# Kernel tuning notes

Measured on AMD Instinct MI355X. Metric: run time of the kernel, lower is better.

The kernel has to match this reference:

```python
import jax, jax.numpy as jnp
import numpy as np

N = 8192       # nodes per graph
E = 262144     # edges per graph (avg degree 32)
D_IN, D_H, D_OUT = 128, 256, 64


def _gcn_layer(x, src, dst, W, b, n):
    # PyG GCNConv: add self-loops, symmetric normalization D^-1/2 (A+I) D^-1/2, then + bias
    xw = x @ W
    loop = jnp.arange(n)
    src_f = jnp.concatenate([src, loop])
    dst_f = jnp.concatenate([dst, loop])
    deg = jax.ops.segment_sum(jnp.ones(src_f.shape[0], x.dtype), dst_f, num_segments=n)
    dinv = jax.lax.rsqrt(jnp.maximum(deg, jnp.asarray(1e-12, x.dtype)))
    norm = dinv[src_f] * dinv[dst_f]                      # [E+N]
    msg = xw[src_f] * norm[:, None]                       # gather + scale
    return jax.ops.segment_sum(msg, dst_f, num_segments=n) + b


def _cross_attn(x1, x2, q, k, v):
    Q = x1 @ q
    V = x1 @ v
    K = x2 @ k
    e = jax.nn.leaky_relu(Q @ K.T, negative_slope=0.01)  # [N1, N2]
    attn = jax.nn.softmax(e, axis=-1)
    return attn @ V


def setup_inputs() -> dict:
    key = jax.random.key(0)
    ks = jax.random.split(key, 20)
    std = 1.0 / np.sqrt(D_OUT)

    def gw(k, shape, fan_in):
        return jax.random.normal(k, shape, jnp.float32) * (1.0 / np.sqrt(fan_in))

    def uw(k, shape):
        return jax.random.uniform(k, shape, jnp.float32, -std, std)

    inp = {
        'graph_set1': jax.random.randint(ks[0], (2, E), 0, N),
        'graph_set2': jax.random.randint(ks[1], (2, E), 0, N),
        'x_set1': jax.random.normal(ks[2], (N, D_IN), jnp.float32),
        'x_set2': jax.random.normal(ks[3], (N, D_IN), jnp.float32),
        'W11': gw(ks[4], (D_IN, D_H), D_IN),  'b11': jnp.zeros((D_H,), jnp.float32),
        'W12': gw(ks[5], (D_H, D_OUT), D_H),  'b12': jnp.zeros((D_OUT,), jnp.float32),
        'W21': gw(ks[6], (D_IN, D_H), D_IN),  'b21': jnp.zeros((D_H,), jnp.float32),
        'W22': gw(ks[7], (D_H, D_OUT), D_H),  'b22': jnp.zeros((D_OUT,), jnp.float32),
        'q1': uw(ks[8], (D_OUT, D_OUT)), 'k1': uw(ks[9], (D_OUT, D_OUT)), 'v1': uw(ks[10], (D_OUT, D_OUT)),
        'q2': uw(ks[11], (D_OUT, D_OUT)), 'k2': uw(ks[12], (D_OUT, D_OUT)), 'v2': uw(ks[13], (D_OUT, D_OUT)),
    }
    return inp


def reference(graph_set1, graph_set2, x_set1, x_set2,
              W11, b11, W12, b12, W21, b21, W22, b22,
              q1, k1, v1, q2, k2, v2):
    s1, d1 = graph_set1[0], graph_set1[1]
    s2, d2 = graph_set2[0], graph_set2[1]
    # GCN branch 1
    h1 = jax.nn.relu(_gcn_layer(x_set1, s1, d1, W11, b11, N))
    h1 = _gcn_layer(h1, s1, d1, W12, b12, N)
    # GCN branch 2
    h2 = jax.nn.relu(_gcn_layer(x_set2, s2, d2, W21, b21, N))
    h2 = _gcn_layer(h2, s2, d2, W22, b22, N)
    # cross attention fusion (note cross2 consumes the updated out_set1)
    o1 = _cross_attn(h1, h2, q1, k1, v1)
    o2 = _cross_attn(h2, o1, q2, k2, v2)
    logits = (o1 @ o2.T).ravel()                          # [N*N]
    return logits
```

## Files before the change

### kernel.cpp

```cpp
#include <hip/hip_runtime.h>
#include <math.h>

static constexpr int NN = 8192;
static constexpr int NE = 262144;
static constexpr int NCH = 8;
static constexpr int NS = (NN / NCH) / 32;

typedef short bfrag __attribute__((ext_vector_type(8)));
typedef float f32x4 __attribute__((ext_vector_type(4)));

#define MFMA(a, b, c) __builtin_amdgcn_mfma_f32_16x16x32_bf16((a), (b), (c), 0, 0, 0)

__device__ __forceinline__ unsigned short f2bf(float x) {
  union { float f; unsigned u; } v; v.f = x;
  unsigned r = v.u + 0x7fffu + ((v.u >> 16) & 1u);
  return (unsigned short)(r >> 16);
}
__device__ __forceinline__ float bf2f(unsigned short h) {
  union { unsigned u; float f; } v; v.u = ((unsigned)h) << 16;
  return v.f;
}

__device__ __forceinline__ void gll16(const void* g, void* l) {
  __builtin_amdgcn_global_load_lds(
      (const __attribute__((address_space(1))) unsigned*)g,
      (__attribute__((address_space(3))) unsigned*)l, 16, 0, 0);
}


__global__ void k_count2(const int* __restrict__ d1, const int* __restrict__ d2,
                         int* __restrict__ i1, int* __restrict__ i2) {
  int t = blockIdx.x * 256 + threadIdx.x;
  const int* d = blockIdx.y ? d2 : d1;
  int* ii = blockIdx.y ? i2 : i1;
  if (t < NE) atomicAdd(&ii[d[t]], 1);
}

__global__ void k_scan2(const int* __restrict__ ideg1, int* __restrict__ off1,
                        int* __restrict__ cur1, float* __restrict__ dinv1,
                        const int* __restrict__ ideg2, int* __restrict__ off2,
                        int* __restrict__ cur2, float* __restrict__ dinv2) {
  const int* indeg = blockIdx.x ? ideg2 : ideg1;
  int* off = blockIdx.x ? off2 : off1;
  int* cur = blockIdx.x ? cur2 : cur1;
  float* dinv = blockIdx.x ? dinv2 : dinv1;
  __shared__ int sh[1024];
  __shared__ int carry;
  int t = threadIdx.x;
  if (t == 0) carry = 0;
  __syncthreads();
  for (int base = 0; base < NN; base += 1024) {
    int v = indeg[base + t];
    sh[t] = v;
    __syncthreads();
    for (int s = 1; s < 1024; s <<= 1) {
      int add = (t >= s) ? sh[t - s] : 0;
      __syncthreads();
      sh[t] += add;
      __syncthreads();
    }
    int excl = carry + sh[t] - v;
    off[base + t] = excl;
    cur[base + t] = excl;
    dinv[base + t] = 1.0f / sqrtf((float)(v + 1));
    __syncthreads();
    if (t == 1023) carry += sh[t];
    __syncthreads();
  }
  if (t == 0) off[NN] = carry;
}

__global__ void k_fill2(const int* __restrict__ s1, const int* __restrict__ d1,
                        int* __restrict__ c1, int* __restrict__ l1,
                        const int* __restrict__ s2, const int* __restrict__ d2,
                        int* __restrict__ c2, int* __restrict__ l2) {
  int t = blockIdx.x * 256 + threadIdx.x;
  const int* src = blockIdx.y ? s2 : s1;
  const int* dst = blockIdx.y ? d2 : d1;
  int* cur = blockIdx.y ? c2 : c1;
  int* out = blockIdx.y ? l2 : l1;
  if (t < NE) {
    int d = dst[t];
    int slot = atomicAdd(&cur[d], 1);
    out[slot] = src[t];
  }
}


__global__ void k_split_w(const float* W11, const float* W21, const float* W12,
                          const float* W22, const float* q1, const float* k1,
                          const float* v1, const float* q2, const float* k2,
                          const float* v2, short* __restrict__ whi,
                          short* __restrict__ wlo) {
  int y = blockIdx.y;
  const float* src; int R, C, base;
  if (y == 0)      { src = W11; R = 128; C = 256; base = 0; }
  else if (y == 1) { src = W21; R = 128; C = 256; base = 32768; }
  else if (y == 2) { src = W12; R = 256; C = 64;  base = 65536; }
  else if (y == 3) { src = W22; R = 256; C = 64;  base = 81920; }
  else if (y == 4) { src = q1;  R = 64;  C = 64;  base = 98304; }
  else if (y == 5) { src = k1;  R = 64;  C = 64;  base = 102400; }
  else if (y == 6) { src = v1;  R = 64;  C = 64;  base = 106496; }
  else if (y == 7) { src = q2;  R = 64;  C = 64;  base = 110592; }
  else if (y == 8) { src = k2;  R = 64;  C = 64;  base = 114688; }
  else             { src = v2;  R = 64;  C = 64;  base = 118784; }
  int idx = blockIdx.x * 256 + threadIdx.x;
  if (idx >= R * C) return;
  int r = idx / C, c = idx % C;
  float x = src[idx];
  unsigned short h = f2bf(x);
  whi[base + c * R + r] = (short)h;
  wlo[base + c * R + r] = (short)f2bf(x - bf2f(h));
}


__global__ __launch_bounds__(256) void k_agg1(const float* __restrict__ x,
                                              const int* __restrict__ off,
                                              const int* __restrict__ srcl,
                                              const float* __restrict__ dinv,
                                              short* __restrict__ ahi,
                                              short* __restrict__ alo) {
  int wave = threadIdx.x >> 6, lane = threadIdx.x & 63;
  int node = blockIdx.x * 4 + wave;
  float dn = dinv[node];
  const float2* xr = (const float2*)x;
  float ax, ay;
  { float2 v = xr[(size_t)node * 64 + lane]; ax = dn * v.x; ay = dn * v.y; }
  int p = off[node], e = off[node + 1];
  for (; p + 3 < e; p += 4) {
    int s0 = srcl[p], s1 = srcl[p + 1], s2 = srcl[p + 2], s3 = srcl[p + 3];
    float w0 = dinv[s0], w1 = dinv[s1], w2 = dinv[s2], w3 = dinv[s3];
    float2 v0 = xr[(size_t)s0 * 64 + lane], v1 = xr[(size_t)s1 * 64 + lane];
    float2 v2 = xr[(size_t)s2 * 64 + lane], v3 = xr[(size_t)s3 * 64 + lane];
    ax += w0 * v0.x + w1 * v1.x + w2 * v2.x + w3 * v3.x;
    ay += w0 * v0.y + w1 * v1.y + w2 * v2.y + w3 * v3.y;
  }
  for (; p < e; ++p) {
    int s = srcl[p];
    float w = dinv[s];
    float2 v = xr[(size_t)s * 64 + lane];
    ax += w * v.x; ay += w * v.y;
  }
  float ox = dn * ax, oy = dn * ay;
  unsigned short hx = f2bf(ox), hy = f2bf(oy);
  int o = node * 128 + lane * 2;
  *(short2*)(ahi + o) = make_short2((short)hx, (short)hy);
  *(short2*)(alo + o) = make_short2((short)f2bf(ox - bf2f(hx)),
                                    (short)f2bf(oy - bf2f(hy)));
}


__global__ __launch_bounds__(256) void k_agg2(const float* __restrict__ t,
                                              const int* __restrict__ off,
                                              const int* __restrict__ srcl,
                                              const float* __restrict__ dinv,
                                              const float* __restrict__ bias,
                                              short* __restrict__ ghi,
                                              short* __restrict__ glo) {
  int wave = threadIdx.x >> 6, lane = threadIdx.x & 63;
  int node = blockIdx.x * 4 + wave;
  float dn = dinv[node];
  float acc = dn * t[(size_t)node * 64 + lane];
  int p = off[node], e = off[node + 1];
  for (; p + 3 < e; p += 4) {
    int s0 = srcl[p], s1 = srcl[p + 1], s2 = srcl[p + 2], s3 = srcl[p + 3];
    float w0 = dinv[s0], w1 = dinv[s1], w2 = dinv[s2], w3 = dinv[s3];
    acc += w0 * t[(size_t)s0 * 64 + lane] + w1 * t[(size_t)s1 * 64 + lane] +
           w2 * t[(size_t)s2 * 64 + lane] + w3 * t[(size_t)s3 * 64 + lane];
  }
  for (; p < e; ++p) {
    int s = srcl[p];
    acc += dinv[s] * t[(size_t)s * 64 + lane];
  }
  float o = dn * acc + bias[lane];
  unsigned short h = f2bf(o);
  ghi[(size_t)node * 64 + lane] = (short)h;
  glo[(size_t)node * 64 + lane] = (short)f2bf(o - bf2f(h));
}


template <int K, int NTOT, bool BIAS, bool RELU, bool OUTHL>
__global__ __launch_bounds__(64) void k_gemm_mfma(
    const short* __restrict__ Ahi, const short* __restrict__ Alo,
    const short* __restrict__ Bthi, const short* __restrict__ Btlo,
    const float* __restrict__ bias, short* __restrict__ Chi,
    short* __restrict__ Clo, float* __restrict__ Cf) {
  constexpr int KS = K / 32;
  int lane = threadIdx.x;
  int lo16 = lane & 15, hi4 = lane >> 4;
  int r0 = blockIdx.x * 16;
  int c0 = blockIdx.y * 64;
  bfrag ah[KS], al[KS];
  const char* abh = (const char*)Ahi + ((size_t)(r0 + lo16) * K + hi4 * 8) * 2;
  const char* abl = (const char*)Alo + ((size_t)(r0 + lo16) * K + hi4 * 8) * 2;
#pragma unroll
  for (int ks = 0; ks < KS; ++ks) {
    ah[ks] = *(const bfrag*)(abh + ks * 64);
    al[ks] = *(const bfrag*)(abl + ks * 64);
  }
  f32x4 z = {0.f, 0.f, 0.f, 0.f};
  f32x4 acc[4] = {z, z, z, z};
#pragma unroll
  for (int c = 0; c < 4; ++c) {
    const char* bbh = (const char*)Bthi + ((size_t)(c0 + c * 16 + lo16) * K + hi4 * 8) * 2;
    const char* bbl = (const char*)Btlo + ((size_t)(c0 + c * 16 + lo16) * K + hi4 * 8) * 2;
#pragma unroll
    for (int ks = 0; ks < KS; ++ks) {
      bfrag bh = *(const bfrag*)(bbh + ks * 64);
      bfrag bl = *(const bfrag*)(bbl + ks * 64);
      acc[c] = MFMA(ah[ks], bh, acc[c]);
      acc[c] = MFMA(ah[ks], bl, acc[c]);
      acc[c] = MFMA(al[ks], bh, acc[c]);
    }
  }
#pragma unroll
  for (int c = 0; c < 4; ++c) {
    int col = c0 + c * 16 + lo16;
    float bv = BIAS ? bias[col] : 0.f;
#pragma unroll
    for (int r = 0; r < 4; ++r) {
      int row = r0 + hi4 * 4 + r;
      float v = acc[c][r] + bv;
      if (RELU) v = fmaxf(v, 0.f);
      if (OUTHL) {
        unsigned short h = f2bf(v);
        Chi[(size_t)row * NTOT + col] = (short)h;
        Clo[(size_t)row * NTOT + col] = (short)f2bf(v - bf2f(h));
      } else {
        Cf[(size_t)row * NTOT + col] = v;
      }
    }
  }
}


__global__ __launch_bounds__(64) void k_qkv(
    const short* __restrict__ Aqhi, const short* __restrict__ Aqlo,
    const short* __restrict__ Akhi, const short* __restrict__ Aklo,
    const short* __restrict__ Avhi, const short* __restrict__ Avlo,
    const short* __restrict__ whi, const short* __restrict__ wlo,
    int bq, int bk, int bv,
    short* __restrict__ Qhi, short* __restrict__ Qlo,
    short* __restrict__ Khi, short* __restrict__ Klo, float* __restrict__ Vf) {
  int y = blockIdx.y;
  const short *Ah, *Al;
  int boff;
  if (y == 0)      { Ah = Aqhi; Al = Aqlo; boff = bq; }
  else if (y == 1) { Ah = Akhi; Al = Aklo; boff = bk; }
  else             { Ah = Avhi; Al = Avlo; boff = bv; }
  const short* Bh = whi + boff;
  const short* Bl = wlo + boff;
  int lane = threadIdx.x;
  int lo16 = lane & 15, hi4 = lane >> 4;
  int r0 = blockIdx.x * 16;
  bfrag ah0, ah1, al0, al1;
  {
    const char* a = (const char*)(Ah + (size_t)(r0 + lo16) * 64 + hi4 * 8);
    const char* b = (const char*)(Al + (size_t)(r0 + lo16) * 64 + hi4 * 8);
    ah0 = *(const bfrag*)a; ah1 = *(const bfrag*)(a + 64);
    al0 = *(const bfrag*)b; al1 = *(const bfrag*)(b + 64);
  }
  f32x4 z = {0.f, 0.f, 0.f, 0.f};
  f32x4 acc[4] = {z, z, z, z};
#pragma unroll
  for (int c = 0; c < 4; ++c) {
    const char* bbh = (const char*)(Bh + (size_t)(c * 16 + lo16) * 64 + hi4 * 8);
    const char* bbl = (const char*)(Bl + (size_t)(c * 16 + lo16) * 64 + hi4 * 8);
    bfrag bh0 = *(const bfrag*)bbh, bh1 = *(const bfrag*)(bbh + 64);
    bfrag bl0 = *(const bfrag*)bbl, bl1 = *(const bfrag*)(bbl + 64);
    acc[c] = MFMA(ah0, bh0, acc[c]);
    acc[c] = MFMA(ah1, bh1, acc[c]);
    acc[c] = MFMA(ah0, bl0, acc[c]);
    acc[c] = MFMA(ah1, bl1, acc[c]);
    acc[c] = MFMA(al0, bh0, acc[c]);
    acc[c] = MFMA(al1, bh1, acc[c]);
  }
#pragma unroll
  for (int c = 0; c < 4; ++c) {
    int col = c * 16 + lo16;
#pragma unroll
    for (int r = 0; r < 4; ++r) {
      int row = r0 + hi4 * 4 + r;
      float v = acc[c][r];
      if (y == 2) {
        Vf[(size_t)row * 64 + col] = v;
      } else {
        unsigned short h = f2bf(v);
        short* oh = (y == 0) ? Qhi : Khi;
        short* ol = (y == 0) ? Qlo : Klo;
        oh[(size_t)row * 64 + col] = (short)h;
        ol[(size_t)row * 64 + col] = (short)f2bf(v - bf2f(h));
      }
    }
  }
}

__global__ __launch_bounds__(256) void k_split_tr(const float* __restrict__ V,
                                                  short* __restrict__ Vthi,
                                                  short* __restrict__ Vtlo) {
  __shared__ float tile[64][65];
  int n0 = blockIdx.x * 64;
  int c = threadIdx.x & 63;
  int rb = threadIdx.x >> 6;
  for (int r = rb; r < 64; r += 4) tile[r][c] = V[(size_t)(n0 + r) * 64 + c];
  __syncthreads();
  for (int r = rb; r < 64; r += 4) {
    float x = tile[c][r];
    unsigned short h = f2bf(x);
    Vthi[(size_t)r * NN + n0 + c] = (short)h;
    Vtlo[(size_t)r * NN + n0 + c] = (short)f2bf(x - bf2f(h));
  }
}


__global__ __launch_bounds__(256) void k_attn_v3(
    const short* __restrict__ Qhi, const short* __restrict__ Qlo,
    const short* __restrict__ Khi_g, const short* __restrict__ Klo_g,
    const short* __restrict__ Vthi_g, const short* __restrict__ Vtlo_g,
    float* __restrict__ Opart, float* __restrict__ mpart, float* __restrict__ lpart) {
  __shared__ short skh[2][32 * 64], skl[2][32 * 64];
  __shared__ short svh[2][64 * 32], svl[2][64 * 32];
  __shared__ short plds[4][16 * 40];
  const int tid = threadIdx.x;
  const int wave = tid >> 6, lane = tid & 63;
  const int lo16 = lane & 15, hi4 = lane >> 4;
  const int q0 = blockIdx.x * 64 + wave * 16;
  const int j0 = blockIdx.y * (NN / NCH);
  short* myp = plds[wave];

  const int krow = wave * 8 + (lane >> 3);
  const int kcbs = ((lane & 7) * 16) ^ ((krow & 7) << 4);
  const int vrow = wave * 16 + (lane >> 2);
  const int vcbs = ((lane & 3) * 16) ^ (((vrow >> 1) & 3) << 4);
  const char* gkh = (const char*)Khi_g + (size_t)(j0 + krow) * 128 + kcbs;
  const char* gkl = (const char*)Klo_g + (size_t)(j0 + krow) * 128 + kcbs;
  const char* gvh = (const char*)Vthi_g + (size_t)vrow * (NN * 2) + (size_t)j0 * 2 + vcbs;
  const char* gvl = (const char*)Vtlo_g + (size_t)vrow * (NN * 2) + (size_t)j0 * 2 + vcbs;

#define STAGE(buf, s)                                             \
  do {                                                            \
    gll16(gkh + (size_t)(s) * 4096, (char*)skh[buf] + wave * 1024); \
    gll16(gkl + (size_t)(s) * 4096, (char*)skl[buf] + wave * 1024); \
    gll16(gvh + (s) * 64, (char*)svh[buf] + wave * 1024);           \
    gll16(gvl + (s) * 64, (char*)svl[buf] + wave * 1024);           \
  } while (0)

  const bfrag* qph = (const bfrag*)(Qhi + (size_t)(q0 + lo16) * 64 + hi4 * 8);
  const bfrag* qpl = (const bfrag*)(Qlo + (size_t)(q0 + lo16) * 64 + hi4 * 8);
  bfrag qh0 = qph[0], qh1 = qph[4];
  bfrag ql0 = qpl[0], ql1 = qpl[4];

  f32x4 z = {0.f, 0.f, 0.f, 0.f};
  f32x4 oacc[4] = {z, z, z, z};
  float mrun[4] = {-1e30f, -1e30f, -1e30f, -1e30f};
  float lsum[4] = {0.f, 0.f, 0.f, 0.f};

  STAGE(0, 0);
  __syncthreads();

  for (int s = 0; s < NS; ++s) {
    const int buf = s & 1;
    if (s + 1 < NS) STAGE(buf ^ 1, s + 1);
    const char* kh = (const char*)skh[buf];
    const char* kl = (const char*)skl[buf];
    f32x4 sa[2];
#pragma unroll
    for (int t = 0; t < 2; ++t) {
      int jr = 16 * t + lo16;
      int sw = (jr & 7) << 4;
      const char* rowh = kh + jr * 128;
      const char* rowl = kl + jr * 128;
      bfrag kh0 = *(const bfrag*)(rowh + ((hi4 * 16) ^ sw));
      bfrag kh1 = *(const bfrag*)(rowh + ((64 + hi4 * 16) ^ sw));
      bfrag kl0 = *(const bfrag*)(rowl + ((hi4 * 16) ^ sw));
      bfrag kl1 = *(const bfrag*)(rowl + ((64 + hi4 * 16) ^ sw));
      f32x4 acc = z;
      acc = MFMA(qh0, kh0, acc);
      acc = MFMA(qh1, kh1, acc);
      acc = MFMA(qh0, kl0, acc);
      acc = MFMA(qh1, kl1, acc);
      acc = MFMA(ql0, kh0, acc);
      acc = MFMA(ql1, kh1, acc);
      sa[t] = acc;
    }
#pragma unroll
    for (int t = 0; t < 2; ++t)
#pragma unroll
      for (int r = 0; r < 4; ++r) {
        float v = sa[t][r];
        sa[t][r] = fmaxf(v, 0.01f * v);
      }
    float pm[4];
#pragma unroll
    for (int r = 0; r < 4; ++r) pm[r] = fmaxf(sa[0][r], sa[1][r]);
#pragma unroll
    for (int mask = 1; mask <= 8; mask <<= 1)
#pragma unroll
      for (int r = 0; r < 4; ++r) pm[r] = fmaxf(pm[r], __shfl_xor(pm[r], mask));
    bool rb = false;
#pragma unroll
    for (int r = 0; r < 4; ++r) rb |= (pm[r] > mrun[r] + 4.f);
    if (__any(rb)) {
#pragma unroll
      for (int r = 0; r < 4; ++r) {
        float nm = (pm[r] > mrun[r] + 4.f) ? pm[r] : mrun[r];
        float c_ = __expf(mrun[r] - nm);
        lsum[r] *= c_;
#pragma unroll
        for (int c = 0; c < 4; ++c) oacc[c][r] *= c_;
        mrun[r] = nm;
      }
    }
    float p0[4], p1[4];
#pragma unroll
    for (int r = 0; r < 4; ++r) {
      p0[r] = __expf(sa[0][r] - mrun[r]);
      p1[r] = __expf(sa[1][r] - mrun[r]);
      lsum[r] += p0[r] + p1[r];
    }
#pragma unroll
    for (int r = 0; r < 4; ++r) {
      int row = hi4 * 4 + r;
      myp[row * 40 + lo16] = (short)f2bf(p0[r]);
      myp[row * 40 + 16 + lo16] = (short)f2bf(p1[r]);
    }
    bfrag pa = *(const bfrag*)(myp + lo16 * 40 + hi4 * 8);
    const char* vh = (const char*)svh[buf];
    const char* vl = (const char*)svl[buf];
#pragma unroll
    for (int c = 0; c < 4; ++c) {
      int dv = 16 * c + lo16;
      int svw = ((dv >> 1) & 3) << 4;
      bfrag vhf = *(const bfrag*)(vh + dv * 64 + ((hi4 * 16) ^ svw));
      bfrag vlf = *(const bfrag*)(vl + dv * 64 + ((hi4 * 16) ^ svw));
      oacc[c] = MFMA(pa, vhf, oacc[c]);
      oacc[c] = MFMA(pa, vlf, oacc[c]);
    }
    __syncthreads();
  }
#undef STAGE
#pragma unroll
  for (int mask = 1; mask <= 8; mask <<= 1)
#pragma unroll
    for (int r = 0; r < 4; ++r) lsum[r] += __shfl_xor(lsum[r], mask);
#pragma unroll
  for (int c = 0; c < 4; ++c)
#pragma unroll
    for (int r = 0; r < 4; ++r)
      Opart[((size_t)blockIdx.y * NN + q0 + hi4 * 4 + r) * 64 + 16 * c + lo16] = oacc[c][r];
  if (lo16 == 0) {
#pragma unroll
    for (int r = 0; r < 4; ++r) {
      mpart[blockIdx.y * NN + q0 + hi4 * 4 + r] = mrun[r];
      lpart[blockIdx.y * NN + q0 + hi4 * 4 + r] = lsum[r];
    }
  }
}

__global__ void k_comb(const float* __restrict__ Opart,
                       const float* __restrict__ mpart,
                       const float* __restrict__ lpart,
                       short* __restrict__ Ohi, short* __restrict__ Olo) {
  int row = blockIdx.x * 4 + (threadIdx.x >> 6);
  int d = threadIdx.x & 63;
  float M = -1e30f;
  for (int i = 0; i < NCH; ++i) M = fmaxf(M, mpart[i * NN + row]);
  float L = 0.f, acc = 0.f;
  for (int i = 0; i < NCH; ++i) {
    float w = __expf(mpart[i * NN + row] - M);
    L += w * lpart[i * NN + row];
    acc += w * Opart[((size_t)i * NN + row) * 64 + d];
  }
  float o = acc / L;
  unsigned short h = f2bf(o);
  Ohi[(size_t)row * 64 + d] = (short)h;
  Olo[(size_t)row * 64 + d] = (short)f2bf(o - bf2f(h));
}


__global__ __launch_bounds__(256) void k_outer(const short* __restrict__ o1hi,
                                               const short* __restrict__ o1lo,
                                               const short* __restrict__ o2hi,
                                               const short* __restrict__ o2lo,
                                               float* __restrict__ out) {
  int wave = threadIdx.x >> 6, lane = threadIdx.x & 63;
  int lo16 = lane & 15, hi4 = lane >> 4;
  int i0 = blockIdx.x * 64 + wave * 16;
  const bfrag* aph = (const bfrag*)(o1hi + (size_t)(i0 + lo16) * 64 + hi4 * 8);
  const bfrag* apl = (const bfrag*)(o1lo + (size_t)(i0 + lo16) * 64 + hi4 * 8);
  bfrag ah0 = aph[0], ah1 = aph[4];
  bfrag al0 = apl[0], al1 = apl[4];
  f32x4 z = {0.f, 0.f, 0.f, 0.f};
  int jbase = blockIdx.y * (NN / 16);

#define LOADB(JV, BH0, BH1, BL0, BL1)                                        \
  do {                                                                       \
    const bfrag* bph = (const bfrag*)(o2hi + (size_t)((JV) + lo16) * 64 + hi4 * 8); \
    const bfrag* bpl = (const bfrag*)(o2lo + (size_t)((JV) + lo16) * 64 + hi4 * 8); \
    BH0 = bph[0]; BH1 = bph[4]; BL0 = bpl[0]; BL1 = bpl[4];                  \
  } while (0)

#define COMP(JV, BH0, BH1, BL0, BL1)                                  \
  do {                                                                \
    f32x4 acc = z;                                                    \
    acc = MFMA(ah0, BH0, acc);                                        \
    acc = MFMA(ah1, BH1, acc);                                        \
    acc = MFMA(ah0, BL0, acc);                                        \
    acc = MFMA(ah1, BL1, acc);                                        \
    acc = MFMA(al0, BH0, acc);                                        \
    acc = MFMA(al1, BH1, acc);                                        \
    _Pragma("unroll")                                                 \
    for (int r = 0; r < 4; ++r)                                       \
      out[(size_t)(i0 + hi4 * 4 + r) * NN + (JV) + lo16] = acc[r];    \
  } while (0)

  bfrag pah0, pah1, pal0, pal1, pbh0, pbh1, pbl0, pbl1;
  LOADB(jbase, pah0, pah1, pal0, pal1);
  for (int jt = 0; jt < NN / 16 / 16; jt += 2) {
    int ja = jbase + jt * 16;
    LOADB(ja + 16, pbh0, pbh1, pbl0, pbl1);
    COMP(ja, pah0, pah1, pal0, pal1);
    if (jt + 2 < NN / 16 / 16) LOADB(ja + 32, pah0, pah1, pal0, pal1);
    COMP(ja + 16, pbh0, pbh1, pbl0, pbl1);
  }
#undef LOADB
#undef COMP
}


extern "C" void kernel_launch(void* const* d_in, const int* in_sizes, int n_in,
                              void* d_out, int out_size, void* d_ws, size_t ws_size,
                              hipStream_t stream) {
  const int* g1 = (const int*)d_in[0];
  const int* g2 = (const int*)d_in[1];
  const float* x1 = (const float*)d_in[2];
  const float* x2 = (const float*)d_in[3];
  const float* W11 = (const float*)d_in[4];
  const float* b11 = (const float*)d_in[5];
  const float* W12 = (const float*)d_in[6];
  const float* b12 = (const float*)d_in[7];
  const float* W21 = (const float*)d_in[8];
  const float* b21 = (const float*)d_in[9];
  const float* W22 = (const float*)d_in[10];
  const float* b22 = (const float*)d_in[11];
  const float* q1 = (const float*)d_in[12];
  const float* k1 = (const float*)d_in[13];
  const float* v1 = (const float*)d_in[14];
  const float* q2 = (const float*)d_in[15];
  const float* k2 = (const float*)d_in[16];
  const float* v2 = (const float*)d_in[17];

  char* ob = (char*)d_out;
  const size_t MB = 1u << 20;
  int* srcl1 = (int*)(ob + 0 * MB);
  int* srcl2 = (int*)(ob + 1 * MB);
  char* small = ob + 2 * MB;
  int* ideg1 = (int*)(small);
  int* ideg2 = (int*)(small + (32u << 10));
  int* off1 = (int*)(small + (64u << 10));
  int* off2 = (int*)(small + (128u << 10));
  int* cur1 = (int*)(small + (192u << 10));
  int* cur2 = (int*)(small + (256u << 10));
  float* dinv1 = (float*)(small + (320u << 10));
  float* dinv2 = (float*)(small + (384u << 10));
  short* whi = (short*)(ob + 3 * MB);
  short* wlo = (short*)(ob + 3 * MB + (512u << 10));
  short* a1hi = (short*)(ob + 4 * MB);
  short* a1lo = (short*)(ob + 6 * MB);
  short* a2hi = (short*)(ob + 8 * MB);
  short* a2lo = (short*)(ob + 10 * MB);
  short* h1hi = (short*)(ob + 12 * MB);
  short* h1lo = (short*)(ob + 16 * MB);
  short* h2hi = (short*)(ob + 20 * MB);
  short* h2lo = (short*)(ob + 24 * MB);
  float* tbuf = (float*)(ob + 28 * MB);
  short* g1hi = (short*)(ob + 30 * MB);
  short* g1lo = (short*)(ob + 31 * MB);
  short* g2hi = (short*)(ob + 32 * MB);
  short* g2lo = (short*)(ob + 33 * MB);
  short* Qhi = (short*)(ob + 34 * MB);
  short* Qlo = (short*)(ob + 35 * MB);
  short* Khi = (short*)(ob + 36 * MB);
  short* Klo = (short*)(ob + 37 * MB);
  float* Vf = (float*)(ob + 38 * MB);
  short* Vthi = (short*)(ob + 40 * MB);
  short* Vtlo = (short*)(ob + 41 * MB);
  float* Opart = (float*)(ob + 42 * MB);
  float* mpart = (float*)(ob + 58 * MB);
  float* lpart = (float*)(ob + 58 * MB + (256u << 10));
  short* o1hi = (short*)d_ws;
  short* o1lo = (short*)((char*)d_ws + 1 * MB);
  short* o2hi = (short*)((char*)d_ws + 2 * MB);
  short* o2lo = (short*)((char*)d_ws + 3 * MB);

  hipMemsetAsync(ideg1, 0, 64u << 10, stream);
  k_count2<<<dim3(1024, 2), 256, 0, stream>>>(g1 + NE, g2 + NE, ideg1, ideg2);
  k_scan2<<<2, 1024, 0, stream>>>(ideg1, off1, cur1, dinv1, ideg2, off2, cur2, dinv2);
  k_fill2<<<dim3(1024, 2), 256, 0, stream>>>(g1, g1 + NE, cur1, srcl1,
                                             g2, g2 + NE, cur2, srcl2);
  k_split_w<<<dim3(128, 10), 256, 0, stream>>>(W11, W21, W12, W22, q1, k1, v1,
                                               q2, k2, v2, whi, wlo);

  k_agg1<<<2048, 256, 0, stream>>>(x1, off1, srcl1, dinv1, a1hi, a1lo);
  k_gemm_mfma<128, 256, true, true, true><<<dim3(512, 4), 64, 0, stream>>>(
      a1hi, a1lo, whi + 0, wlo + 0, b11, h1hi, h1lo, nullptr);
  k_gemm_mfma<256, 64, false, false, false><<<dim3(512, 1), 64, 0, stream>>>(
      h1hi, h1lo, whi + 65536, wlo + 65536, nullptr, nullptr, nullptr, tbuf);
  k_agg2<<<2048, 256, 0, stream>>>(tbuf, off1, srcl1, dinv1, b12, g1hi, g1lo);
  k_agg1<<<2048, 256, 0, stream>>>(x2, off2, srcl2, dinv2, a2hi, a2lo);
  k_gemm_mfma<128, 256, true, true, true><<<dim3(512, 4), 64, 0, stream>>>(
      a2hi, a2lo, whi + 32768, wlo + 32768, b21, h2hi, h2lo, nullptr);
  k_gemm_mfma<256, 64, false, false, false><<<dim3(512, 1), 64, 0, stream>>>(
      h2hi, h2lo, whi + 81920, wlo + 81920, nullptr, nullptr, nullptr, tbuf);
  k_agg2<<<2048, 256, 0, stream>>>(tbuf, off2, srcl2, dinv2, b22, g2hi, g2lo);

  k_qkv<<<dim3(512, 3), 64, 0, stream>>>(g1hi, g1lo, g2hi, g2lo, g1hi, g1lo,
                                         whi, wlo, 98304, 102400, 106496,
                                         Qhi, Qlo, Khi, Klo, Vf);
  k_split_tr<<<128, 256, 0, stream>>>(Vf, Vthi, Vtlo);
  k_attn_v3<<<dim3(128, NCH), 256, 0, stream>>>(Qhi, Qlo, Khi, Klo, Vthi, Vtlo,
                                                Opart, mpart, lpart);
  k_comb<<<2048, 256, 0, stream>>>(Opart, mpart, lpart, o1hi, o1lo);

  k_qkv<<<dim3(512, 3), 64, 0, stream>>>(g2hi, g2lo, o1hi, o1lo, g2hi, g2lo,
                                         whi, wlo, 110592, 114688, 118784,
                                         Qhi, Qlo, Khi, Klo, Vf);
  k_split_tr<<<128, 256, 0, stream>>>(Vf, Vthi, Vtlo);
  k_attn_v3<<<dim3(128, NCH), 256, 0, stream>>>(Qhi, Qlo, Khi, Klo, Vthi, Vtlo,
                                                Opart, mpart, lpart);
  k_comb<<<2048, 256, 0, stream>>>(Opart, mpart, lpart, o2hi, o2lo);

  k_outer<<<dim3(128, 16), 256, 0, stream>>>(o1hi, o1lo, o2hi, o2lo, (float*)d_out);

  (void)in_sizes; (void)n_in; (void)out_size; (void)ws_size;
}
```

Before: 764.8 us.

## Batch both GCN branches per launch, fuse V transpose into QKV, widen attention blocks

Each GCN stage (aggregation and both GEMM layers) now processes both graph branches in a single launch using a grid dimension to pick the branch, which halves the launch count and fills more of the GPU per launch. The V projection now writes the transposed hi/lo bf16 split directly, which removes the separate k_split_tr kernel and its fp32 round trip. The attention kernel uses 512-thread blocks covering 128 queries. Waves 0-3 load K tiles and waves 4-7 load V tiles, so each staged K/V tile is shared by twice as many queries. The costs are more register and LDS pressure per block and short4 strided stores into Vt.

New measurement: 718.9 us. 6.0% less time.

```diff
diff --git a/kernel.cpp b/kernel.cpp
--- a/kernel.cpp
+++ b/kernel.cpp
@@ -114,12 +114,20 @@
 }
 
 
-__global__ __launch_bounds__(256) void k_agg1(const float* __restrict__ x,
-                                              const int* __restrict__ off,
-                                              const int* __restrict__ srcl,
-                                              const float* __restrict__ dinv,
-                                              short* __restrict__ ahi,
-                                              short* __restrict__ alo) {
+__global__ __launch_bounds__(256) void k_agg1d(
+    const float* __restrict__ x1, const float* __restrict__ x2,
+    const int* __restrict__ off1, const int* __restrict__ srcl1,
+    const float* __restrict__ dinv1, const int* __restrict__ off2,
+    const int* __restrict__ srcl2, const float* __restrict__ dinv2,
+    short* __restrict__ a1hi, short* __restrict__ a1lo,
+    short* __restrict__ a2hi, short* __restrict__ a2lo) {
+  int br = blockIdx.y;
+  const float* x = br ? x2 : x1;
+  const int* off = br ? off2 : off1;
+  const int* srcl = br ? srcl2 : srcl1;
+  const float* dinv = br ? dinv2 : dinv1;
+  short* ahi = br ? a2hi : a1hi;
+  short* alo = br ? a2lo : a1lo;
   int wave = threadIdx.x >> 6, lane = threadIdx.x & 63;
   int node = blockIdx.x * 4 + wave;
   float dn = dinv[node];
@@ -150,13 +158,22 @@
 }
 
 
-__global__ __launch_bounds__(256) void k_agg2(const float* __restrict__ t,
-                                              const int* __restrict__ off,
-                                              const int* __restrict__ srcl,
-                                              const float* __restrict__ dinv,
-                                              const float* __restrict__ bias,
-                                              short* __restrict__ ghi,
-                                              short* __restrict__ glo) {
+__global__ __launch_bounds__(256) void k_agg2d(
+    const float* __restrict__ t1, const float* __restrict__ t2,
+    const int* __restrict__ off1, const int* __restrict__ srcl1,
+    const float* __restrict__ dinv1, const int* __restrict__ off2,
+    const int* __restrict__ srcl2, const float* __restrict__ dinv2,
+    const float* __restrict__ b12, const float* __restrict__ b22,
+    short* __restrict__ g1hi, short* __restrict__ g1lo,
+    short* __restrict__ g2hi, short* __restrict__ g2lo) {
+  int br = blockIdx.y;
+  const float* t = br ? t2 : t1;
+  const int* off = br ? off2 : off1;
+  const int* srcl = br ? srcl2 : srcl1;
+  const float* dinv = br ? dinv2 : dinv1;
+  const float* bias = br ? b22 : b12;
+  short* ghi = br ? g2hi : g1hi;
+  short* glo = br ? g2lo : g1lo;
   int wave = threadIdx.x >> 6, lane = threadIdx.x & 63;
   int node = blockIdx.x * 4 + wave;
   float dn = dinv[node];
@@ -179,22 +196,30 @@
 }
 
 
-template <int K, int NTOT, bool BIAS, bool RELU, bool OUTHL>
-__global__ __launch_bounds__(64) void k_gemm_mfma(
-    const short* __restrict__ Ahi, const short* __restrict__ Alo,
-    const short* __restrict__ Bthi, const short* __restrict__ Btlo,
-    const float* __restrict__ bias, short* __restrict__ Chi,
-    short* __restrict__ Clo, float* __restrict__ Cf) {
-  constexpr int KS = K / 32;
+__global__ __launch_bounds__(64) void k_gemmL1(
+    const short* __restrict__ a1hi, const short* __restrict__ a1lo,
+    const short* __restrict__ a2hi, const short* __restrict__ a2lo,
+    const short* __restrict__ whi, const short* __restrict__ wlo,
+    const float* __restrict__ b11, const float* __restrict__ b21,
+    short* __restrict__ h1hi, short* __restrict__ h1lo,
+    short* __restrict__ h2hi, short* __restrict__ h2lo) {
+  int br = blockIdx.z;
+  const short* Ahi = br ? a2hi : a1hi;
+  const short* Alo = br ? a2lo : a1lo;
+  const short* Bh = whi + (br ? 32768 : 0);
+  const short* Bl = wlo + (br ? 32768 : 0);
+  const float* bias = br ? b21 : b11;
+  short* Chi = br ? h2hi : h1hi;
+  short* Clo = br ? h2lo : h1lo;
   int lane = threadIdx.x;
   int lo16 = lane & 15, hi4 = lane >> 4;
   int r0 = blockIdx.x * 16;
   int c0 = blockIdx.y * 64;
-  bfrag ah[KS], al[KS];
-  const char* abh = (const char*)Ahi + ((size_t)(r0 + lo16) * K + hi4 * 8) * 2;
-  const char* abl = (const char*)Alo + ((size_t)(r0 + lo16) * K + hi4 * 8) * 2;
-#pragma unroll
-  for (int ks = 0; ks < KS; ++ks) {
+  bfrag ah[4], al[4];
+  const char* abh = (const char*)Ahi + ((size_t)(r0 + lo16) * 128 + hi4 * 8) * 2;
+  const char* abl = (const char*)Alo + ((size_t)(r0 + lo16) * 128 + hi4 * 8) * 2;
+#pragma unroll
+  for (int ks = 0; ks < 4; ++ks) {
     ah[ks] = *(const bfrag*)(abh + ks * 64);
     al[ks] = *(const bfrag*)(abl + ks * 64);
   }
@@ -202,10 +227,10 @@
   f32x4 acc[4] = {z, z, z, z};
 #pragma unroll
   for (int c = 0; c < 4; ++c) {
-    const char* bbh = (const char*)Bthi + ((size_t)(c0 + c * 16 + lo16) * K + hi4 * 8) * 2;
-    const char* bbl = (const char*)Btlo + ((size_t)(c0 + c * 16 + lo16) * K + hi4 * 8) * 2;
-#pragma unroll
-    for (int ks = 0; ks < KS; ++ks) {
+    const char* bbh = (const char*)Bh + ((size_t)(c0 + c * 16 + lo16) * 128 + hi4 * 8) * 2;
+    const char* bbl = (const char*)Bl + ((size_t)(c0 + c * 16 + lo16) * 128 + hi4 * 8) * 2;
+#pragma unroll
+    for (int ks = 0; ks < 4; ++ks) {
       bfrag bh = *(const bfrag*)(bbh + ks * 64);
       bfrag bl = *(const bfrag*)(bbl + ks * 64);
       acc[c] = MFMA(ah[ks], bh, acc[c]);
@@ -216,20 +241,62 @@
 #pragma unroll
   for (int c = 0; c < 4; ++c) {
     int col = c0 + c * 16 + lo16;
-    float bv = BIAS ? bias[col] : 0.f;
+    float bv = bias[col];
 #pragma unroll
     for (int r = 0; r < 4; ++r) {
       int row = r0 + hi4 * 4 + r;
-      float v = acc[c][r] + bv;
-      if (RELU) v = fmaxf(v, 0.f);
-      if (OUTHL) {
-        unsigned short h = f2bf(v);
-        Chi[(size_t)row * NTOT + col] = (short)h;
-        Clo[(size_t)row * NTOT + col] = (short)f2bf(v - bf2f(h));
-      } else {
-        Cf[(size_t)row * NTOT + col] = v;
-      }
-    }
+      float v = fmaxf(acc[c][r] + bv, 0.f);
+      unsigned short h = f2bf(v);
+      Chi[(size_t)row * 256 + col] = (short)h;
+      Clo[(size_t)row * 256 + col] = (short)f2bf(v - bf2f(h));
+    }
+  }
+}
+
+
+__global__ __launch_bounds__(64) void k_gemmL2(
+    const short* __restrict__ h1hi, const short* __restrict__ h1lo,
+    const short* __restrict__ h2hi, const short* __restrict__ h2lo,
+    const short* __restrict__ whi, const short* __restrict__ wlo,
+    float* __restrict__ t1, float* __restrict__ t2) {
+  int br = blockIdx.y;
+  const short* Ahi = br ? h2hi : h1hi;
+  const short* Alo = br ? h2lo : h1lo;
+  const short* Bh = whi + (br ? 81920 : 65536);
+  const short* Bl = wlo + (br ? 81920 : 65536);
+  float* Cf = br ? t2 : t1;
+  int lane = threadIdx.x;
+  int lo16 = lane & 15, hi4 = lane >> 4;
+  int r0 = blockIdx.x * 16;
+  bfrag ah[8], al[8];
+  const char* abh = (const char*)Ahi + ((size_t)(r0 + lo16) * 256 + hi4 * 8) * 2;
+  const char* abl = (const char*)Alo + ((size_t)(r0 + lo16) * 256 + hi4 * 8) * 2;
+#pragma unroll
+  for (int ks = 0; ks < 8; ++ks) {
+    ah[ks] = *(const bfrag*)(abh + ks * 64);
+    al[ks] = *(const bfrag*)(abl + ks * 64);
+  }
+  f32x4 z = {0.f, 0.f, 0.f, 0.f};
+  f32x4 acc[4] = {z, z, z, z};
+#pragma unroll
+  for (int c = 0; c < 4; ++c) {
+    const char* bbh = (const char*)Bh + ((size_t)(c * 16 + lo16) * 256 + hi4 * 8) * 2;
+    const char* bbl = (const char*)Bl + ((size_t)(c * 16 + lo16) * 256 + hi4 * 8) * 2;
+#pragma unroll
+    for (int ks = 0; ks < 8; ++ks) {
+      bfrag bh = *(const bfrag*)(bbh + ks * 64);
+      bfrag bl = *(const bfrag*)(bbl + ks * 64);
+      acc[c] = MFMA(ah[ks], bh, acc[c]);
+      acc[c] = MFMA(ah[ks], bl, acc[c]);
+      acc[c] = MFMA(al[ks], bh, acc[c]);
+    }
+  }
+#pragma unroll
+  for (int c = 0; c < 4; ++c) {
+    int col = c * 16 + lo16;
+#pragma unroll
+    for (int r = 0; r < 4; ++r)
+      Cf[(size_t)(r0 + hi4 * 4 + r) * 64 + col] = acc[c][r];
   }
 }
 
@@ -241,7 +308,8 @@
     const short* __restrict__ whi, const short* __restrict__ wlo,
     int bq, int bk, int bv,
     short* __restrict__ Qhi, short* __restrict__ Qlo,
-    short* __restrict__ Khi, short* __restrict__ Klo, float* __restrict__ Vf) {
+    short* __restrict__ Khi, short* __restrict__ Klo,
+    short* __restrict__ Vthi, short* __restrict__ Vtlo) {
   int y = blockIdx.y;
   const short *Ah, *Al;
   int boff;
@@ -275,19 +343,31 @@
     acc[c] = MFMA(al0, bh0, acc[c]);
     acc[c] = MFMA(al1, bh1, acc[c]);
   }
-#pragma unroll
-  for (int c = 0; c < 4; ++c) {
-    int col = c * 16 + lo16;
-#pragma unroll
-    for (int r = 0; r < 4; ++r) {
-      int row = r0 + hi4 * 4 + r;
-      float v = acc[c][r];
-      if (y == 2) {
-        Vf[(size_t)row * 64 + col] = v;
-      } else {
+  if (y == 2) {
+#pragma unroll
+    for (int c = 0; c < 4; ++c) {
+      int col = c * 16 + lo16;
+      short4 vh, vl;
+      float v0 = acc[c][0], v1 = acc[c][1], v2 = acc[c][2], v3 = acc[c][3];
+      unsigned short h0 = f2bf(v0), h1 = f2bf(v1), h2 = f2bf(v2), h3 = f2bf(v3);
+      vh = make_short4((short)h0, (short)h1, (short)h2, (short)h3);
+      vl = make_short4((short)f2bf(v0 - bf2f(h0)), (short)f2bf(v1 - bf2f(h1)),
+                       (short)f2bf(v2 - bf2f(h2)), (short)f2bf(v3 - bf2f(h3)));
+      size_t o = (size_t)col * NN + r0 + hi4 * 4;
+      *(short4*)(Vthi + o) = vh;
+      *(short4*)(Vtlo + o) = vl;
+    }
+  } else {
+    short* oh = (y == 0) ? Qhi : Khi;
+    short* ol = (y == 0) ? Qlo : Klo;
+#pragma unroll
+    for (int c = 0; c < 4; ++c) {
+      int col = c * 16 + lo16;
+#pragma unroll
+      for (int r = 0; r < 4; ++r) {
+        int row = r0 + hi4 * 4 + r;
+        float v = acc[c][r];
         unsigned short h = f2bf(v);
-        short* oh = (y == 0) ? Qhi : Khi;
-        short* ol = (y == 0) ? Qlo : Klo;
         oh[(size_t)row * 64 + col] = (short)h;
         ol[(size_t)row * 64 + col] = (short)f2bf(v - bf2f(h));
       }
@@ -295,54 +375,41 @@
   }
 }
 
-__global__ __launch_bounds__(256) void k_split_tr(const float* __restrict__ V,
-                                                  short* __restrict__ Vthi,
-                                                  short* __restrict__ Vtlo) {
-  __shared__ float tile[64][65];
-  int n0 = blockIdx.x * 64;
-  int c = threadIdx.x & 63;
-  int rb = threadIdx.x >> 6;
-  for (int r = rb; r < 64; r += 4) tile[r][c] = V[(size_t)(n0 + r) * 64 + c];
-  __syncthreads();
-  for (int r = rb; r < 64; r += 4) {
-    float x = tile[c][r];
-    unsigned short h = f2bf(x);
-    Vthi[(size_t)r * NN + n0 + c] = (short)h;
-    Vtlo[(size_t)r * NN + n0 + c] = (short)f2bf(x - bf2f(h));
-  }
-}
-
-
-__global__ __launch_bounds__(256) void k_attn_v3(
+
+__global__ __launch_bounds__(512) void k_attn_v4(
     const short* __restrict__ Qhi, const short* __restrict__ Qlo,
     const short* __restrict__ Khi_g, const short* __restrict__ Klo_g,
     const short* __restrict__ Vthi_g, const short* __restrict__ Vtlo_g,
     float* __restrict__ Opart, float* __restrict__ mpart, float* __restrict__ lpart) {
   __shared__ short skh[2][32 * 64], skl[2][32 * 64];
   __shared__ short svh[2][64 * 32], svl[2][64 * 32];
-  __shared__ short plds[4][16 * 40];
+  __shared__ short plds[8][16 * 40];
   const int tid = threadIdx.x;
   const int wave = tid >> 6, lane = tid & 63;
   const int lo16 = lane & 15, hi4 = lane >> 4;
-  const int q0 = blockIdx.x * 64 + wave * 16;
+  const int q0 = blockIdx.x * 128 + wave * 16;
   const int j0 = blockIdx.y * (NN / NCH);
+  const int wv = wave & 3;
   short* myp = plds[wave];
 
-  const int krow = wave * 8 + (lane >> 3);
+  const int krow = wv * 8 + (lane >> 3);
   const int kcbs = ((lane & 7) * 16) ^ ((krow & 7) << 4);
-  const int vrow = wave * 16 + (lane >> 2);
+  const int vrow = wv * 16 + (lane >> 2);
   const int vcbs = ((lane & 3) * 16) ^ (((vrow >> 1) & 3) << 4);
-  const char* gkh = (const char*)Khi_g + (size_t)(j0 + krow) * 128 + kcbs;
-  const char* gkl = (const char*)Klo_g + (size_t)(j0 + krow) * 128 + kcbs;
-  const char* gvh = (const char*)Vthi_g + (size_t)vrow * (NN * 2) + (size_t)j0 * 2 + vcbs;
-  const char* gvl = (const char*)Vtlo_g + (size_t)vrow * (NN * 2) + (size_t)j0 * 2 + vcbs;
-
-#define STAGE(buf, s)                                             \
-  do {                                                            \
-    gll16(gkh + (size_t)(s) * 4096, (char*)skh[buf] + wave * 1024); \
-    gll16(gkl + (size_t)(s) * 4096, (char*)skl[buf] + wave * 1024); \
-    gll16(gvh + (s) * 64, (char*)svh[buf] + wave * 1024);           \
-    gll16(gvl + (s) * 64, (char*)svl[buf] + wave * 1024);           \
+  const char* gka = (const char*)Khi_g + (size_t)(j0 + krow) * 128 + kcbs;
+  const char* gkb = (const char*)Klo_g + (size_t)(j0 + krow) * 128 + kcbs;
+  const char* gva = (const char*)Vthi_g + (size_t)vrow * (NN * 2) + (size_t)j0 * 2 + vcbs;
+  const char* gvb = (const char*)Vtlo_g + (size_t)vrow * (NN * 2) + (size_t)j0 * 2 + vcbs;
+
+#define STAGE(buf, s)                                                \
+  do {                                                               \
+    if (wave < 4) {                                                  \
+      gll16(gka + (size_t)(s) * 4096, (char*)skh[buf] + wv * 1024);  \
+      gll16(gkb + (size_t)(s) * 4096, (char*)skl[buf] + wv * 1024);  \
+    } else {                                                         \
+      gll16(gva + (s) * 64, (char*)svh[buf] + wv * 1024);            \
+      gll16(gvb + (s) * 64, (char*)svl[buf] + wv * 1024);            \
+    }                                                                \
   } while (0)
 
   const bfrag* qph = (const bfrag*)(Qhi + (size_t)(q0 + lo16) * 64 + hi4 * 8);
@@ -573,16 +640,16 @@
   short* h1lo = (short*)(ob + 16 * MB);
   short* h2hi = (short*)(ob + 20 * MB);
   short* h2lo = (short*)(ob + 24 * MB);
-  float* tbuf = (float*)(ob + 28 * MB);
-  short* g1hi = (short*)(ob + 30 * MB);
-  short* g1lo = (short*)(ob + 31 * MB);
-  short* g2hi = (short*)(ob + 32 * MB);
-  short* g2lo = (short*)(ob + 33 * MB);
-  short* Qhi = (short*)(ob + 34 * MB);
-  short* Qlo = (short*)(ob + 35 * MB);
-  short* Khi = (short*)(ob + 36 * MB);
-  short* Klo = (short*)(ob + 37 * MB);
-  float* Vf = (float*)(ob + 38 * MB);
+  float* tbuf1 = (float*)(ob + 28 * MB);
+  float* tbuf2 = (float*)(ob + 30 * MB);
+  short* g1hi = (short*)(ob + 32 * MB);
+  short* g1lo = (short*)(ob + 33 * MB);
+  short* g2hi = (short*)(ob + 34 * MB);
+  short* g2lo = (short*)(ob + 35 * MB);
+  short* Qhi = (short*)(ob + 36 * MB);
+  short* Qlo = (short*)(ob + 37 * MB);
+  short* Khi = (short*)(ob + 38 * MB);
+  short* Klo = (short*)(ob + 39 * MB);
   short* Vthi = (short*)(ob + 40 * MB);
   short* Vtlo = (short*)(ob + 41 * MB);
   float* Opart = (float*)(ob + 42 * MB);
@@ -601,33 +668,29 @@
   k_split_w<<<dim3(128, 10), 256, 0, stream>>>(W11, W21, W12, W22, q1, k1, v1,
                                                q2, k2, v2, whi, wlo);
 
-  k_agg1<<<2048, 256, 0, stream>>>(x1, off1, srcl1, dinv1, a1hi, a1lo);
-  k_gemm_mfma<128, 256, true, true, true><<<dim3(512, 4), 64, 0, stream>>>(
-      a1hi, a1lo, whi + 0, wlo + 0, b11, h1hi, h1lo, nullptr);
-  k_gemm_mfma<256, 64, false, false, false><<<dim3(512, 1), 64, 0, stream>>>(
-      h1hi, h1lo, whi + 65536, wlo + 65536, nullptr, nullptr, nullptr, tbuf);
-  k_agg2<<<2048, 256, 0, stream>>>(tbuf, off1, srcl1, dinv1, b12, g1hi, g1lo);
-  k_agg1<<<2048, 256, 0, stream>>>(x2, off2, srcl2, dinv2, a2hi, a2lo);
-  k_gemm_mfma<128, 256, true, true, true><<<dim3(512, 4), 64, 0, stream>>>(
-      a2hi, a2lo, whi + 32768, wlo + 32768, b21, h2hi, h2lo, nullptr);
-  k_gemm_mfma<256, 64, false, false, false><<<dim3(512, 1), 64, 0, stream>>>(
-      h2hi, h2lo, whi + 81920, wlo + 81920, nullptr, nullptr, nullptr, tbuf);
-  k_agg2<<<2048, 256, 0, stream>>>(tbuf, off2, srcl2, dinv2, b22, g2hi, g2lo);
+  k_agg1d<<<dim3(2048, 2), 256, 0, stream>>>(x1, x2, off1, srcl1, dinv1,
+                                             off2, srcl2, dinv2,
+                                             a1hi, a1lo, a2hi, a2lo);
+  k_gemmL1<<<dim3(512, 4, 2), 64, 0, stream>>>(a1hi, a1lo, a2hi, a2lo, whi, wlo,
+                                               b11, b21, h1hi, h1lo, h2hi, h2lo);
+  k_gemmL2<<<dim3(512, 2), 64, 0, stream>>>(h1hi, h1lo, h2hi, h2lo, whi, wlo,
+                                            tbuf1, tbuf2);
+  k_agg2d<<<dim3(2048, 2), 256, 0, stream>>>(tbuf1, tbuf2, off1, srcl1, dinv1,
+                                             off2, srcl2, dinv2, b12, b22,
+                                             g1hi, g1lo, g2hi, g2lo);
 
   k_qkv<<<dim3(512, 3), 64, 0, stream>>>(g1hi, g1lo, g2hi, g2lo, g1hi, g1lo,
                                          whi, wlo, 98304, 102400, 106496,
-                                         Qhi, Qlo, Khi, Klo, Vf);
-  k_split_tr<<<128, 256, 0, stream>>>(Vf, Vthi, Vtlo);
-  k_attn_v3<<<dim3(128, NCH), 256, 0, stream>>>(Qhi, Qlo, Khi, Klo, Vthi, Vtlo,
-                                                Opart, mpart, lpart);
+                                         Qhi, Qlo, Khi, Klo, Vthi, Vtlo);
+  k_attn_v4<<<dim3(64, NCH), 512, 0, stream>>>(Qhi, Qlo, Khi, Klo, Vthi, Vtlo,
+                                               Opart, mpart, lpart);
   k_comb<<<2048, 256, 0, stream>>>(Opart, mpart, lpart, o1hi, o1lo);
 
   k_qkv<<<dim3(512, 3), 64, 0, stream>>>(g2hi, g2lo, o1hi, o1lo, g2hi, g2lo,
                                          whi, wlo, 110592, 114688, 118784,
-                                         Qhi, Qlo, Khi, Klo, Vf);
-  k_split_tr<<<128, 256, 0, stream>>>(Vf, Vthi, Vtlo);
-  k_attn_v3<<<dim3(128, NCH), 256, 0, stream>>>(Qhi, Qlo, Khi, Klo, Vthi, Vtlo,
-                                                Opart, mpart, lpart);
+                                         Qhi, Qlo, Khi, Klo, Vthi, Vtlo);
+  k_attn_v4<<<dim3(64, NCH), 512, 0, stream>>>(Qhi, Qlo, Khi, Klo, Vthi, Vtlo,
+                                               Opart, mpart, lpart);
   k_comb<<<2048, 256, 0, stream>>>(Opart, mpart, lpart, o2hi, o2lo);
 
   k_outer<<<dim3(128, 16), 256, 0, stream>>>(o1hi, o1lo, o2hi, o2lo, (float*)d_out);
```
